# Kernel tuning notes

Hardware: AMD Instinct MI355X
Metric: run time of the kernel (lower is better)

## Reference

```python
import jax, jax.numpy as jnp
import numpy as np

# ViT-B on the Lorentz hyperboloid (curvature C): points x = [x_time, x_space],
# x_time = sqrt(||x_space||^2 + C). All linear/conv/norm ops act on the space
# part and recompute time; residuals/attention-midpoints renormalize the full
# Lorentz vector back onto the hyperboloid.
B, IMG, P, CIN, D, H, L = 32, 224, 16, 3, 768, 12, 12
HD = D // H          # per-head space dim (64)
DFF = 2048           # swiglu hidden: int(2/3 * 4*768) aligned to 64
C = 1.0
EPS = 1e-6


def _time(xs):
    return jnp.sqrt(jnp.clip(jnp.sum(xs * xs, -1, keepdims=True) + C, EPS, None))


def _to_lorentz(xs):
    return jnp.concatenate([_time(xs), xs], -1)


def _project(z):
    # renormalize full Lorentz vector so <z,z>_L = -C
    zz = jnp.sum(z[..., 1:] ** 2, -1, keepdims=True) - z[..., :1] ** 2
    return z * (jnp.sqrt(C) / jnp.sqrt(jnp.clip(-zz, EPS, None)))


def _lorentz_ln(x, g, b):
    xs = x[..., 1:]
    mu = xs.mean(-1, keepdims=True)
    var = ((xs - mu) ** 2).mean(-1, keepdims=True)
    xs = (xs - mu) / jnp.sqrt(var + 1e-6) * g + b
    return _to_lorentz(xs)


def _lresnet(x, y, w):
    # Lorentzian weighted residual: midpoint of x and w*y, projected to manifold
    return _project(x + w * y)


def _rope_tables():
    # 2D axial rope over the 14x14 patch grid, identity rotation for 1 cls token
    n = IMG // P
    d4 = HD // 4
    inv = 1.0 / (100.0 ** (np.arange(d4) / d4))
    ang = np.arange(n)[:, None] * inv[None, :]            # [n, d4]
    ay = np.repeat(ang[:, None, :], n, axis=1)            # row angles
    ax = np.repeat(ang[None, :, :], n, axis=0)            # col angles
    a = np.concatenate([ay, ax], -1).reshape(n * n, HD // 2)
    cos = np.concatenate([np.ones((1, HD // 2)), np.cos(a)], 0)
    sin = np.concatenate([np.zeros((1, HD // 2)), np.sin(a)], 0)
    return jnp.asarray(cos, jnp.float32), jnp.asarray(sin, jnp.float32)


def _apply_rope(x, cos, sin):
    # x: [B,N,H,HD]; rotate consecutive pairs (complex multiply)
    xr = x.reshape(*x.shape[:-1], -1, 2)
    x0, x1 = xr[..., 0], xr[..., 1]
    c = cos[None, :, None, :]
    s = sin[None, :, None, :]
    out = jnp.stack([x0 * c - x1 * s, x0 * s + x1 * c], -1)
    return out.reshape(x.shape)


def _attention(x, Wq, Wk, Wv, Wo, cos, sin, scale):
    b, n, _ = x.shape
    xs = x[..., 1:]
    q = (xs @ Wq).reshape(b, n, H, HD)
    k = (xs @ Wk).reshape(b, n, H, HD)
    v = (xs @ Wv).reshape(b, n, H, HD)
    q = _apply_rope(q, cos, sin)
    k = _apply_rope(k, cos, sin)
    qt = _time(q)[..., 0]   # [B,N,H]
    kt = _time(k)[..., 0]
    # Lorentz inner product <q,k>_L = -q_t k_t + q_s . k_s
    inner = jnp.einsum('bnhd,bmhd->bhnm', q, k) - jnp.einsum('bnh,bmh->bhnm', qt, kt)
    attn = jax.nn.softmax((2.0 * C + 2.0 * inner) / scale, axis=-1)
    vf = jnp.concatenate([_time(v), v], -1)               # [B,M,H,HD+1]
    mid = jnp.einsum('bhnm,bmhe->bnhe', attn, vf)         # Lorentzian midpoint
    mid = _project(mid)
    out_s = mid[..., 1:].reshape(b, n, H * HD) @ Wo       # concat heads + proj
    return _to_lorentz(out_s)


def setup_inputs() -> dict:
    key = jax.random.key(0)
    ks = jax.random.split(key, 12)
    std = 0.02
    nrm = lambda k, shape: jax.random.normal(k, shape, jnp.float32) * std
    return {
        'x': jax.random.normal(ks[0], (B, CIN, IMG, IMG), jnp.float32),
        'cls_s': nrm(ks[1], (D - 1,)),
        'Wp': nrm(ks[2], (P, P, CIN + 1, D - 1)),         # HWIO conv kernel
        'ln1_g': jnp.ones((L, D - 1), jnp.float32),
        'ln1_b': jnp.zeros((L, D - 1), jnp.float32),
        'Wq': nrm(ks[3], (L, D - 1, H * HD)),
        'Wk': nrm(ks[4], (L, D - 1, H * HD)),
        'Wv': nrm(ks[5], (L, D - 1, H * HD)),
        'Wo': nrm(ks[6], (L, H * HD, D - 1)),
        'ln2_g': jnp.ones((L, D - 1), jnp.float32),
        'ln2_b': jnp.zeros((L, D - 1), jnp.float32),
        'W1': nrm(ks[7], (L, D - 1, DFF)),
        'W2': nrm(ks[8], (L, D - 1, DFF)),
        'W3': nrm(ks[9], (L, DFF, D - 1)),
        'wy1': jnp.ones((L,), jnp.float32),
        'wy2': jnp.ones((L,), jnp.float32),
        'lnf_g': jnp.ones((D - 1,), jnp.float32),
        'lnf_b': jnp.zeros((D - 1,), jnp.float32),
    }


def reference(x, cls_s, Wp, ln1_g, ln1_b, Wq, Wk, Wv, Wo, ln2_g, ln2_b,
              W1, W2, W3, wy1, wy2, lnf_g, lnf_b):
    b = x.shape[0]
    xs = jnp.transpose(x, (0, 2, 3, 1))                   # BHWC
    xl = _to_lorentz(xs)                                  # pixel-wise time channel
    feat = jax.lax.conv_general_dilated(
        xl, Wp, (P, P), 'VALID',
        dimension_numbers=('NHWC', 'HWIO', 'NHWC'))       # [B,14,14,D-1]
    tok = _to_lorentz(feat).reshape(b, -1, D)             # [B,196,D]
    cls = jnp.broadcast_to(_to_lorentz(cls_s)[None, None, :], (b, 1, D))
    tok = jnp.concatenate([cls, tok], 1)                  # [B,197,D]
    cos, sin = _rope_tables()
    scale = jnp.sqrt(jnp.asarray(H * HD, jnp.float32))
    for l in range(L):
        xn = _lorentz_ln(tok, ln1_g[l], ln1_b[l])
        a = _attention(xn, Wq[l], Wk[l], Wv[l], Wo[l], cos, sin, scale)
        tok = _lresnet(tok, a, wy1[l])
        xn = _lorentz_ln(tok, ln2_g[l], ln2_b[l])
        hs = xn[..., 1:]
        m = _to_lorentz((jax.nn.silu(hs @ W1[l]) * (hs @ W2[l])) @ W3[l])
        tok = _lresnet(tok, m, wy2[l])
    return _lorentz_ln(tok, lnf_g, lnf_b)
```

## Files before the change

kernel.cpp:

```cpp
#include <hip/hip_runtime.h>
#include <hip/hip_bf16.h>

typedef __attribute__((ext_vector_type(8))) short short8;
typedef __attribute__((ext_vector_type(4))) float f32x4;
typedef _Float16 f16x8 __attribute__((ext_vector_type(8)));

#define NLAYER 12
#define NTOK   6304
#define MPAD   6400
#define CONVM  6272

#define QELE     ((size_t)384*208*64)
#define VELE     ((size_t)384*80*232)

static constexpr size_t AL(size_t x){ return (x + 511) & ~(size_t)511; }
static constexpr size_t B_COS    = 0;
static constexpr size_t B_SIN    = AL(B_COS    + (size_t)197*32*4);
static constexpr size_t B_WPT    = AL(B_SIN    + (size_t)197*32*4);
static constexpr size_t B_APATCH = AL(B_WPT    + (size_t)768*1024*2);
static constexpr size_t B_WQKVT  = AL(B_APATCH + (size_t)CONVM*1024*2);
static constexpr size_t B_WOT    = AL(B_WQKVT  + (size_t)2304*768*2);
static constexpr size_t B_W12T   = AL(B_WOT    + (size_t)768*768*2);
static constexpr size_t B_W3T    = AL(B_W12T   + (size_t)4096*768*2);
static constexpr size_t B_TOK    = AL(B_W3T    + (size_t)768*2048*2);
static constexpr size_t B_ACTA   = AL(B_TOK    + (size_t)NTOK*768*4);
static constexpr size_t B_ACTB   = AL(B_ACTA   + (size_t)MPAD*768*2);
static constexpr size_t B_GOUT   = AL(B_ACTB   + (size_t)MPAD*2048*2);
static constexpr size_t B_QB     = AL(B_GOUT   + (size_t)MPAD*2304*4);
static constexpr size_t B_KB     = AL(B_QB     + QELE*2);
static constexpr size_t B_VT     = AL(B_KB     + QELE*2);
static constexpr size_t B_QTB    = AL(B_VT     + VELE*2);
static constexpr size_t B_KTB    = AL(B_QTB    + (size_t)384*208*4);
static constexpr size_t B_END    = AL(B_KTB    + (size_t)384*208*4);

typedef __attribute__((address_space(1))) unsigned int gu32;
typedef __attribute__((address_space(3))) unsigned int lu32;
__device__ __forceinline__ void gld16(const void* g, void* l) {
  __builtin_amdgcn_global_load_lds((const gu32*)g, (lu32*)l, 16, 0, 0);
}

__device__ __forceinline__ float bsum(float v, float* red) {
  #pragma unroll
  for (int m = 32; m; m >>= 1) v += __shfl_xor(v, m, 64);
  __syncthreads();
  if ((threadIdx.x & 63) == 0) red[threadIdx.x >> 6] = v;
  __syncthreads();
  return red[0] + red[1] + red[2] + red[3];
}

__device__ __forceinline__ ushort h_us(float v) {
  _Float16 h = (_Float16)v;
  return *(ushort*)&h;
}
__device__ __forceinline__ float us_f(ushort u) {
  return (float)*(const _Float16*)&u;
}

__global__ void k_rope_tab(float* __restrict__ cosb, float* __restrict__ sinb) {
  int idx = blockIdx.x * 256 + threadIdx.x;
  if (idx >= 197 * 32) return;
  int p = idx >> 5, j = idx & 31;
  float cv, sv;
  if (p == 0) { cv = 1.f; sv = 0.f; }
  else {
    int pp = p - 1;
    int iy = pp / 14, ix = pp - iy * 14;
    int pos = (j < 16) ? iy : ix;
    int f   = (j < 16) ? j  : j - 16;
    float inv = powf(100.f, -(float)f / 16.f);
    float a = (float)pos * inv;
    cv = cosf(a); sv = sinf(a);
  }
  cosb[idx] = cv; sinb[idx] = sv;
}

__device__ __forceinline__ void tpose_tile(const float* __restrict__ src, ushort* __restrict__ dst,
                                           int K, int N, int ldd, int imode, int tk, int tn) {
  __shared__ float ts[32][33];
  int t = threadIdx.x;
  int rr = t >> 3, c4 = (t & 7) * 4;
  int k0 = tk * 32, n0 = tn * 32;
  #pragma unroll
  for (int e = 0; e < 4; ++e) {
    int k = k0 + rr, n = n0 + c4 + e;
    ts[rr][c4 + e] = (k < K && n < N) ? src[(size_t)k * N + n] : 0.f;
  }
  __syncthreads();
  int c = n0 + rr;
  int drow = (imode == 0) ? c : (16 * (c >> 3) + (c & 7) + (imode == 2 ? 8 : 0));
  ushort4 o;
  #pragma unroll
  for (int e = 0; e < 4; ++e) {
    _Float16 hv = (_Float16)ts[c4 + e][rr];
    ((ushort*)&o)[e] = *(ushort*)&hv;
  }
  *(ushort4*)&dst[(size_t)drow * ldd + k0 + c4] = o;
}

__global__ __launch_bounds__(256) void k_tpose(const float* __restrict__ src, ushort* __restrict__ dst,
                                               int K, int N, int ktiles, int ldd) {
  int tk = blockIdx.x % ktiles, tn = blockIdx.x / ktiles;
  tpose_tile(src, dst, K, N, ldd, 0, tk, tn);
}

__global__ __launch_bounds__(256) void k_wprep(const float* __restrict__ Wq, const float* __restrict__ Wk,
                                               const float* __restrict__ Wv, const float* __restrict__ Wo,
                                               const float* __restrict__ W1, const float* __restrict__ W2,
                                               const float* __restrict__ W3,
                                               ushort* __restrict__ wqkvt, ushort* __restrict__ wot,
                                               ushort* __restrict__ w12t, ushort* __restrict__ w3t) {
  int tile = blockIdx.x;
  const float* src; ushort* dst;
  int K, N, ktiles, ldd, imode = 0, tl;
  if (tile < 2304) {
    int jb = tile / 576; tl = tile % 576;
    ktiles = 24; ldd = 768;
    if (jb == 0)      { src = Wq; dst = wqkvt;                 K = 767; N = 768; }
    else if (jb == 1) { src = Wk; dst = wqkvt + 768 * 768;     K = 767; N = 768; }
    else if (jb == 2) { src = Wv; dst = wqkvt + 2 * 768 * 768; K = 767; N = 768; }
    else              { src = Wo; dst = wot;                   K = 768; N = 767; }
  } else if (tile < 5376) {
    int jb = (tile - 2304) / 1536; tl = (tile - 2304) % 1536;
    ktiles = 24; ldd = 768; K = 767; N = 2048; dst = w12t;
    src = jb ? W2 : W1; imode = jb ? 2 : 1;
  } else {
    tl = tile - 5376; ktiles = 64; ldd = 2048; K = 2048; N = 767; src = W3; dst = w3t;
  }
  int tk = tl % ktiles, tn = tl / ktiles;
  tpose_tile(src, dst, K, N, ldd, imode, tk, tn);
}

__global__ __launch_bounds__(256) void k_im2col(const float* __restrict__ x, ushort* __restrict__ ap) {
  int r = blockIdx.x;
  int b = r / 196, pi = r - b * 196;
  int py = pi / 14, px = pi - py * 14;
  int t = threadIdx.x;
  int ph = t >> 4, pw = t & 15;
  int iy = py * 16 + ph, ix = px * 16 + pw;
  size_t base = ((size_t)b * 3 * 224 + iy) * 224 + ix;
  float x0 = x[base];
  float x1 = x[base + 224 * 224];
  float x2 = x[base + 2 * 224 * 224];
  float tv = sqrtf(fmaxf(x0 * x0 + x1 * x1 + x2 * x2 + 1.f, 1e-6f));
  size_t o = (size_t)r * 1024 + t * 4;
  ap[o] = h_us(tv); ap[o + 1] = h_us(x0); ap[o + 2] = h_us(x1); ap[o + 3] = h_us(x2);
}

template<int MODE>
__global__ __launch_bounds__(256) void k_gemmh(const ushort* __restrict__ A, const ushort* __restrict__ Bt,
                                               float* __restrict__ C, ushort* __restrict__ H,
                                               int N, int K) {
  __shared__ ushort sA[128 * 64];
  __shared__ ushort sB[128 * 64];
  int m0 = blockIdx.x * 128, n0 = blockIdx.y * 128;
  int t = threadIdx.x;
  int w = t >> 6, l = t & 63;
  int wm = (w >> 1) * 64, wn = (w & 1) * 64;
  int lr = l & 15, hi = l >> 4;
  f32x4 acc[4][4] = {};
  for (int k0 = 0; k0 < K; k0 += 64) {
    #pragma unroll
    for (int i = 0; i < 4; ++i) {
      int fl = i * 256 + t;
      int r = fl >> 3, c = fl & 7;
      int cs = c ^ (r & 7);
      gld16(&A[(size_t)(m0 + r) * K + k0 + cs * 8], &sA[fl * 8]);
      gld16(&Bt[(size_t)(n0 + r) * K + k0 + cs * 8], &sB[fl * 8]);
    }
    __syncthreads();
    f16x8 af[4][2], bfr[4][2];
    #pragma unroll
    for (int q = 0; q < 4; ++q) {
      int ra = wm + q * 16 + lr, rb = wn + q * 16 + lr;
      #pragma unroll
      for (int h = 0; h < 2; ++h) {
        af[q][h]  = *(const f16x8*)&sA[ra * 64 + ((h * 4 + hi) ^ (ra & 7)) * 8];
        bfr[q][h] = *(const f16x8*)&sB[rb * 64 + ((h * 4 + hi) ^ (rb & 7)) * 8];
      }
    }
    #pragma unroll
    for (int mi = 0; mi < 4; ++mi)
      #pragma unroll
      for (int ni = 0; ni < 4; ++ni) {
        acc[mi][ni] = __builtin_amdgcn_mfma_f32_16x16x32_f16(af[mi][0], bfr[ni][0], acc[mi][ni], 0, 0, 0);
        acc[mi][ni] = __builtin_amdgcn_mfma_f32_16x16x32_f16(af[mi][1], bfr[ni][1], acc[mi][ni], 0, 0, 0);
      }
    __syncthreads();
  }
  int rr = hi * 4, cc = lr;
  if (MODE == 3) {
    #pragma unroll
    for (int mi = 0; mi < 4; ++mi)
      #pragma unroll
      for (int ni = 0; ni < 4; ++ni)
        #pragma unroll
        for (int j = 0; j < 4; ++j)
          H[(size_t)(m0 + wm + mi * 16 + rr + j) * N + (n0 + wn + ni * 16 + cc)] = h_us(acc[mi][ni][j]);
  } else {
    #pragma unroll
    for (int mi = 0; mi < 4; ++mi)
      #pragma unroll
      for (int ni = 0; ni < 4; ++ni)
        #pragma unroll
        for (int j = 0; j < 4; ++j)
          C[(size_t)(m0 + wm + mi * 16 + rr + j) * N + (n0 + wn + ni * 16 + cc)] = acc[mi][ni][j];
  }
}

template<int MODE>
__global__ __launch_bounds__(512, 2) void k_g256(const ushort* __restrict__ A, const ushort* __restrict__ Bt,
                                                 ushort* __restrict__ H, int N, int K,
                                                 ushort* __restrict__ qbuf, ushort* __restrict__ kbuf,
                                                 ushort* __restrict__ vtb,
                                                 float* __restrict__ qtb, float* __restrict__ ktb,
                                                 const float* __restrict__ cosb, const float* __restrict__ sinb) {
  __shared__ ushort sA[2][2][256 * 32];
  __shared__ ushort sB[2][2][256 * 32];
  const int t = threadIdx.x;
  const int w = t >> 6, l = t & 63;
  const int wr = w >> 2, wc = w & 3;
  const int lr = l & 15, hi4 = l >> 4;
  const int m0 = blockIdx.x * 256, n0 = blockIdx.y * 256;

  auto stageA = [&](int kt, int kh, int buf) {
    #pragma unroll
    for (int ii = 0; ii < 2; ++ii) {
      int q = ii * 512 + t;
      int r = q >> 2, ci = q & 3;
      gld16(&A[(size_t)(m0 + r) * K + kt * 64 + kh * 32 + ((ci ^ ((r >> 1) & 3)) * 8)], &sA[buf][kh][q * 8]);
    }
  };
  auto stageB = [&](int kt, int kh, int buf) {
    #pragma unroll
    for (int ii = 0; ii < 2; ++ii) {
      int q = ii * 512 + t;
      int r = q >> 2, ci = q & 3;
      gld16(&Bt[(size_t)(n0 + r) * K + kt * 64 + kh * 32 + ((ci ^ ((r >> 1) & 3)) * 8)], &sB[buf][kh][q * 8]);
    }
  };

  f32x4 acc[8][4] = {};
  auto ldA = [&](int buf, int ks, int G, f16x8* fr) {
    #pragma unroll
    for (int mi = 0; mi < 4; ++mi) {
      int r = wr * 128 + (G * 4 + mi) * 16 + lr;
      fr[mi] = *(const f16x8*)&sA[buf][ks][(r * 4 + (hi4 ^ ((r >> 1) & 3))) * 8];
    }
  };
  auto ldB = [&](int buf, int ks, f16x8* fr) {
    #pragma unroll
    for (int ni = 0; ni < 4; ++ni) {
      int r = wc * 64 + ni * 16 + lr;
      fr[ni] = *(const f16x8*)&sB[buf][ks][(r * 4 + (hi4 ^ ((r >> 1) & 3))) * 8];
    }
  };
  auto mmaG = [&](int G, f16x8* a, f16x8* b) {
    __builtin_amdgcn_s_setprio(1);
    #pragma unroll
    for (int mi = 0; mi < 4; ++mi)
      #pragma unroll
      for (int ni = 0; ni < 4; ++ni)
        acc[G * 4 + mi][ni] = __builtin_amdgcn_mfma_f32_16x16x32_f16(a[mi], b[ni], acc[G * 4 + mi][ni], 0, 0, 0);
    __builtin_amdgcn_s_setprio(0);
  };

  const int NT = K >> 6;
  const int NI = NT >> 1;
  stageA(0, 0, 0); stageB(0, 0, 0); stageA(0, 1, 0); stageB(0, 1, 0);

  for (int i = 0; i < NI; ++i) {
    const int T1 = 2 * i + 1, T2 = 2 * i + 2;
    const bool last = (i == NI - 1);
    f16x8 a0[4], a1[4], b0[4], b1[4];
    asm volatile("s_waitcnt vmcnt(4)" ::: "memory");
    __builtin_amdgcn_sched_barrier(0);
    __builtin_amdgcn_s_barrier();
    ldA(0, 0, 0, a0); ldB(0, 0, b0);
    stageA(T1, 0, 1);
    mmaG(0, a0, b0);
    ldA(0, 0, 1, a1);
    stageB(T1, 0, 1);
    mmaG(1, a1, b0);
    asm volatile("s_waitcnt vmcnt(4)" ::: "memory");
    __builtin_amdgcn_sched_barrier(0);
    __builtin_amdgcn_s_barrier();
    ldA(0, 1, 0, a0); ldB(0, 1, b1);
    stageA(T1, 1, 1);
    mmaG(0, a0, b1);
    ldA(0, 1, 1, a1);
    stageB(T1, 1, 1);
    mmaG(1, a1, b1);
    asm volatile("s_waitcnt vmcnt(4)" ::: "memory");
    __builtin_amdgcn_sched_barrier(0);
    __builtin_amdgcn_s_barrier();
    ldA(1, 0, 0, a0); ldB(1, 0, b0);
    if (!last) stageA(T2, 0, 0);
    mmaG(0, a0, b0);
    ldA(1, 0, 1, a1);
    if (!last) stageB(T2, 0, 0);
    mmaG(1, a1, b0);
    if (last) { asm volatile("s_waitcnt vmcnt(0)" ::: "memory"); }
    else      { asm volatile("s_waitcnt vmcnt(4)" ::: "memory"); }
    __builtin_amdgcn_sched_barrier(0);
    __builtin_amdgcn_s_barrier();
    ldA(1, 1, 0, a0); ldB(1, 1, b1);
    if (!last) stageA(T2, 1, 0);
    mmaG(0, a0, b1);
    ldA(1, 1, 1, a1);
    if (!last) stageB(T2, 1, 0);
    mmaG(1, a1, b1);
  }

  if (MODE == 1) {
    int cc = lr;
    #pragma unroll
    for (int mi = 0; mi < 8; ++mi)
      #pragma unroll
      for (int ni = 0; ni < 4; ++ni) {
        int g = (n0 + wc * 64 + ni * 16) >> 4;
        #pragma unroll
        for (int j = 0; j < 4; ++j) {
          float v = acc[mi][ni][j];
          float p = __shfl_xor(v, 8);
          float u1 = (cc < 8) ? v : p;
          float u2 = (cc < 8) ? p : v;
          float hv = u1 / (1.f + __expf(-u1)) * u2;
          if (cc < 8)
            H[(size_t)(m0 + wr * 128 + mi * 16 + hi4 * 4 + j) * 2048 + g * 8 + cc] = h_us(hv);
        }
      }
  } else if (MODE == 2) {
    int secBase = n0 + wc * 64;
    int sec = secBase / 768;
    int hh = (secBase - sec * 768) >> 6;
    #pragma unroll
    for (int mi = 0; mi < 8; ++mi) {
      float nrm[4];
      #pragma unroll
      for (int j = 0; j < 4; ++j) {
        float ss = 0.f;
        #pragma unroll
        for (int ni = 0; ni < 4; ++ni) ss += acc[mi][ni][j] * acc[mi][ni][j];
        #pragma unroll
        for (int m = 8; m; m >>= 1) ss += __shfl_xor(ss, m, 64);
        nrm[j] = sqrtf(fmaxf(ss + 1.f, 1e-6f));
      }
      #pragma unroll
      for (int j = 0; j < 4; ++j) {
        int m = m0 + wr * 128 + mi * 16 + hi4 * 4 + j;
        if (m < NTOK) {
          int b = m / 197, nn = m - b * 197;
          int bh = b * 12 + hh;
          if (sec == 2) {
            size_t vo = (size_t)bh * 80 * 232;
            if (lr == 0) vtb[vo + nn] = h_us(nrm[j]);
            #pragma unroll
            for (int ni = 0; ni < 4; ++ni) {
              int e = ni * 16 + lr;
              vtb[vo + (size_t)(1 + e) * 232 + nn] = h_us(acc[mi][ni][j]);
            }
          } else {
            float* tb = (sec == 0) ? qtb : ktb;
            ushort* ob = (sec == 0) ? qbuf : kbuf;
            if (lr == 0) tb[(size_t)bh * 208 + nn] = nrm[j];
            size_t rowb = ((size_t)bh * 208 + nn) * 64;
            #pragma unroll
            for (int ni = 0; ni < 4; ++ni) {
              int d = ni * 16 + lr;
              float v = acc[mi][ni][j];
              float p = __shfl_xor(v, 1);
              int j2 = d >> 1;
              float cz = cosb[nn * 32 + j2], sz = sinb[nn * 32 + j2];
              float rv = ((lr & 1) == 0) ? (v * cz - p * sz) : (p * sz + v * cz);
              ob[rowb + d] = h_us(rv);
            }
          }
        }
      }
    }
  }
}

__global__ __launch_bounds__(256) void k_build_tok(const float* __restrict__ feat, const float* __restrict__ cls,
                                                   float* __restrict__ tok) {
  __shared__ float red[8];
  int r = blockIdx.x;
  int b = r / 197, i = r - b * 197;
  int t = threadIdx.x;
  const float* src = (i == 0) ? cls : (feat + (size_t)(b * 196 + i - 1) * 768);
  float v0 = src[t], v1 = src[256 + t], v2 = (t < 255) ? src[512 + t] : 0.f;
  float qs = bsum(v0 * v0 + v1 * v1 + v2 * v2, red);
  float* tp = tok + (size_t)r * 768;
  if (t == 0) tp[0] = sqrtf(fmaxf(qs + 1.f, 1e-6f));
  tp[1 + t] = v0; tp[257 + t] = v1; if (t < 255) tp[513 + t] = v2;
}

__global__ __launch_bounds__(256) void k_ln(const float* __restrict__ tok, const float* __restrict__ g,
                                            const float* __restrict__ bb, ushort* __restrict__ out) {
  __shared__ float red[8];
  int r = blockIdx.x, t = threadIdx.x;
  const float* xp = tok + (size_t)r * 768;
  float v0 = xp[1 + t], v1 = xp[257 + t], v2 = (t < 255) ? xp[513 + t] : 0.f;
  float s = bsum(v0 + v1 + v2, red);
  float q = bsum(v0 * v0 + v1 * v1 + v2 * v2, red);
  float mu = s * (1.f / 767.f);
  float rstd = rsqrtf(fmaxf(q * (1.f / 767.f) - mu * mu, 0.f) + 1e-6f);
  size_t o = (size_t)r * 768;
  out[o + t]       = h_us((v0 - mu) * rstd * g[t]       + bb[t]);
  out[o + 256 + t] = h_us((v1 - mu) * rstd * g[256 + t] + bb[256 + t]);
  if (t < 255)
    out[o + 512 + t] = h_us((v2 - mu) * rstd * g[512 + t] + bb[512 + t]);
  if (t == 255) out[o + 767] = 0;
}

__global__ __launch_bounds__(128) void k_attn(const ushort* __restrict__ qbuf,
                                              const float* __restrict__ qtb,
                                              const ushort* __restrict__ kbuf,
                                              const float* __restrict__ ktb,
                                              const ushort* __restrict__ vtb,
                                              ushort* __restrict__ outa) {
  __shared__ ushort sK[208 * 72];
  __shared__ ushort sP[2][16 * 248];
  __shared__ float  sKt[208];
  int half = blockIdx.x, bh = blockIdx.y;
  int b = bh / 12, hd = bh - b * 12;
  int t = threadIdx.x, w = t >> 6, l = t & 63;
  const ushort* kg = kbuf + (size_t)bh * 208 * 64;
  for (int cks = t; cks < 1664; cks += 128) {
    int r = cks >> 3, c8 = (cks & 7) * 8;
    *(int4*)&sK[r * 72 + c8] = *(const int4*)&kg[r * 64 + c8];
  }
  for (int i = t; i < 208; i += 128) sKt[i] = ktb[(size_t)bh * 208 + i];
  __syncthreads();
  const ushort* qg = qbuf + (size_t)bh * 208 * 64;
  const ushort* vg = vtb + (size_t)bh * 80 * 232;
  const float invs = 0.03608439182435161f;
  int rt0 = half ? 7 : 0, rt1 = half ? 13 : 7;
  int lr = l & 15, hi4 = l >> 4;
  ushort* pw = &sP[w][0];
  for (int rt = rt0 + w; rt < rt1; rt += 2) {
    int qrow = (rt * 16 + lr) * 64 + hi4 * 8;
    f16x8 q0 = *(const f16x8*)&qg[qrow];
    f16x8 q1 = *(const f16x8*)&qg[qrow + 32];
    float qt4[4];
    #pragma unroll
    for (int j = 0; j < 4; ++j) qt4[j] = qtb[(size_t)bh * 208 + rt * 16 + hi4 * 4 + j];
    f32x4 acc[13];
    #pragma unroll
    for (int nt = 0; nt < 13; ++nt) {
      int kr = (nt * 16 + lr) * 72 + hi4 * 8;
      f16x8 k0 = *(const f16x8*)&sK[kr];
      f16x8 k1 = *(const f16x8*)&sK[kr + 32];
      acc[nt] = (f32x4){0.f, 0.f, 0.f, 0.f};
      acc[nt] = __builtin_amdgcn_mfma_f32_16x16x32_f16(q0, k0, acc[nt], 0, 0, 0);
      acc[nt] = __builtin_amdgcn_mfma_f32_16x16x32_f16(q1, k1, acc[nt], 0, 0, 0);
    }
    float mx[4] = {-1e30f, -1e30f, -1e30f, -1e30f};
    #pragma unroll
    for (int nt = 0; nt < 13; ++nt) {
      int cI = nt * 16 + lr;
      float ktc = sKt[cI];
      bool valid = (cI < 197);
      #pragma unroll
      for (int j = 0; j < 4; ++j) {
        float s = (2.f + 2.f * (acc[nt][j] - qt4[j] * ktc)) * invs;
        acc[nt][j] = s;
        if (valid) mx[j] = fmaxf(mx[j], s);
      }
    }
    #pragma unroll
    for (int j = 0; j < 4; ++j)
      #pragma unroll
      for (int m = 8; m; m >>= 1) mx[j] = fmaxf(mx[j], __shfl_xor(mx[j], m, 64));
    #pragma unroll
    for (int nt = 0; nt < 14; ++nt) {
      int cI = nt * 16 + lr;
      #pragma unroll
      for (int j = 0; j < 4; ++j) {
        float p = (nt < 13 && cI < 197) ? __expf(acc[nt][j] - mx[j]) : 0.f;
        pw[(hi4 * 4 + j) * 248 + cI] = h_us(p);
      }
    }
    f32x4 accO[5];
    #pragma unroll
    for (int et = 0; et < 5; ++et) accO[et] = (f32x4){0.f, 0.f, 0.f, 0.f};
    #pragma unroll
    for (int ks = 0; ks < 7; ++ks) {
      f16x8 pa = *(const f16x8*)&pw[lr * 248 + ks * 32 + hi4 * 8];
      #pragma unroll
      for (int et = 0; et < 5; ++et) {
        int er = et * 16 + lr;
        f16x8 bv = *(const f16x8*)&vg[(er > 64 ? 64 : er) * 232 + ks * 32 + hi4 * 8];
        accO[et] = __builtin_amdgcn_mfma_f32_16x16x32_f16(pa, bv, accO[et], 0, 0, 0);
      }
    }
    float ssq[4] = {0.f, 0.f, 0.f, 0.f};
    #pragma unroll
    for (int et = 0; et < 4; ++et)
      #pragma unroll
      for (int j = 0; j < 4; ++j) ssq[j] += accO[et][j] * accO[et][j];
    if (lr == 0) {
      #pragma unroll
      for (int j = 0; j < 4; ++j) ssq[j] += accO[4][j] * accO[4][j];
    }
    #pragma unroll
    for (int j = 0; j < 4; ++j)
      #pragma unroll
      for (int m = 8; m; m >>= 1) ssq[j] += __shfl_xor(ssq[j], m, 64);
    float rf4[4];
    #pragma unroll
    for (int j = 0; j < 4; ++j) {
      float o0 = __shfl(accO[0][j], (l & 48));
      rf4[j] = rsqrtf(fmaxf(2.f * o0 * o0 - ssq[j], 1e-6f));
    }
    #pragma unroll
    for (int et = 0; et < 5; ++et) {
      int e = et * 16 + lr;
      if (e == 0 || e >= 65) continue;
      #pragma unroll
      for (int j = 0; j < 4; ++j) {
        int n = rt * 16 + hi4 * 4 + j;
        if (n < 197)
          outa[((size_t)(b * 197 + n)) * 768 + hd * 64 + (e - 1)] = h_us(accO[et][j] * rf4[j]);
      }
    }
  }
}

template<int FIN>
__global__ __launch_bounds__(256) void k_resnet_ln(float* __restrict__ tok, const ushort* __restrict__ s,
                                                   const float* __restrict__ wyp, int l,
                                                   const float* __restrict__ g, const float* __restrict__ bb,
                                                   ushort* __restrict__ out16, float* __restrict__ out32) {
  __shared__ float red[8];
  __shared__ float bc[1];
  int r = blockIdx.x, t = threadIdx.x;
  float w = wyp[l];
  const ushort* sp = s + (size_t)r * 768;
  float* tp = tok + (size_t)r * 768;
  float s0 = us_f(sp[t]), s1 = us_f(sp[256 + t]), s2 = (t < 255) ? us_f(sp[512 + t]) : 0.f;
  float qs = bsum(s0 * s0 + s1 * s1 + s2 * s2, red);
  float at = sqrtf(fmaxf(qs + 1.f, 1e-6f));
  float z0 = tp[1 + t] + w * s0;
  float z1 = tp[257 + t] + w * s1;
  float z2 = (t < 255) ? (tp[513 + t] + w * s2) : 0.f;
  float zs = bsum(z0 * z0 + z1 * z1 + z2 * z2, red);
  if (t == 0) bc[0] = tp[0] + w * at;
  __syncthreads();
  float zt = bc[0];
  float rf = rsqrtf(fmaxf(zt * zt - zs, 1e-6f));
  float n0 = z0 * rf, n1 = z1 * rf, n2 = z2 * rf;
  tp[1 + t] = n0; tp[257 + t] = n1; if (t < 255) tp[513 + t] = n2;
  if (t == 0) tp[0] = zt * rf;
  float sm = bsum(n0 + n1 + n2, red);
  float sq = bsum(n0 * n0 + n1 * n1 + n2 * n2, red);
  float mu = sm * (1.f / 767.f);
  float rstd = rsqrtf(fmaxf(sq * (1.f / 767.f) - mu * mu, 0.f) + 1e-6f);
  float y0 = (n0 - mu) * rstd * g[t] + bb[t];
  float y1 = (n1 - mu) * rstd * g[256 + t] + bb[256 + t];
  float y2 = (t < 255) ? ((n2 - mu) * rstd * g[512 + t] + bb[512 + t]) : 0.f;
  if (FIN) {
    float qq = bsum(y0 * y0 + y1 * y1 + y2 * y2, red);
    float* op = out32 + (size_t)r * 768;
    op[1 + t] = y0; op[257 + t] = y1; if (t < 255) op[513 + t] = y2;
    if (t == 0) op[0] = sqrtf(fmaxf(qq + 1.f, 1e-6f));
  } else {
    size_t o = (size_t)r * 768;
    out16[o + t] = h_us(y0);
    out16[o + 256 + t] = h_us(y1);
    if (t < 255) out16[o + 512 + t] = h_us(y2);
    if (t == 255) out16[o + 767] = 0;
  }
}

extern "C" void kernel_launch(void* const* d_in, const int* in_sizes, int n_in,
                              void* d_out, int out_size, void* d_ws, size_t ws_size,
                              hipStream_t stream) {
  const float* x     = (const float*)d_in[0];
  const float* cls_s = (const float*)d_in[1];
  const float* Wp    = (const float*)d_in[2];
  const float* ln1g  = (const float*)d_in[3];
  const float* ln1b  = (const float*)d_in[4];
  const float* Wq    = (const float*)d_in[5];
  const float* Wk    = (const float*)d_in[6];
  const float* Wv    = (const float*)d_in[7];
  const float* Wo    = (const float*)d_in[8];
  const float* ln2g  = (const float*)d_in[9];
  const float* ln2b  = (const float*)d_in[10];
  const float* W1    = (const float*)d_in[11];
  const float* W2    = (const float*)d_in[12];
  const float* W3    = (const float*)d_in[13];
  const float* wy1   = (const float*)d_in[14];
  const float* wy2   = (const float*)d_in[15];
  const float* lnfg  = (const float*)d_in[16];
  const float* lnfb  = (const float*)d_in[17];

  if (ws_size < B_END) return;

  char* ws = (char*)d_ws;
  float*  cosb   = (float*)(ws + B_COS);
  float*  sinb   = (float*)(ws + B_SIN);
  ushort* wpt    = (ushort*)(ws + B_WPT);
  ushort* apatch = (ushort*)(ws + B_APATCH);
  ushort* wqkvt  = (ushort*)(ws + B_WQKVT);
  ushort* wot    = (ushort*)(ws + B_WOT);
  ushort* w12t   = (ushort*)(ws + B_W12T);
  ushort* w3t    = (ushort*)(ws + B_W3T);
  float*  tok    = (float*)(ws + B_TOK);
  ushort* acta   = (ushort*)(ws + B_ACTA);
  ushort* actb   = (ushort*)(ws + B_ACTB);
  float*  gout   = (float*)(ws + B_GOUT);
  ushort* gouth  = (ushort*)(ws + B_GOUT);
  ushort* qbuf   = (ushort*)(ws + B_QB);
  ushort* kbuf   = (ushort*)(ws + B_KB);
  ushort* vtb    = (ushort*)(ws + B_VT);
  float*  qtb    = (float*)(ws + B_QTB);
  float*  ktb    = (float*)(ws + B_KTB);

  hipMemsetAsync(vtb, 0, VELE * 2, stream);

  k_rope_tab<<<25, 256, 0, stream>>>(cosb, sinb);
  k_tpose<<<32 * 24, 256, 0, stream>>>(Wp, wpt, 1024, 767, 32, 1024);
  k_im2col<<<CONVM, 256, 0, stream>>>(x, apatch);
  k_gemmh<0><<<dim3(49, 6), 256, 0, stream>>>(apatch, wpt, gout, nullptr, 768, 1024);
  k_build_tok<<<NTOK, 256, 0, stream>>>(gout, cls_s, tok);
  k_ln<<<NTOK, 256, 0, stream>>>(tok, ln1g, ln1b, acta);

  for (int l = 0; l < NLAYER; ++l) {
    k_wprep<<<6912, 256, 0, stream>>>(Wq + (size_t)l * 767 * 768, Wk + (size_t)l * 767 * 768,
                                      Wv + (size_t)l * 767 * 768, Wo + (size_t)l * 768 * 767,
                                      W1 + (size_t)l * 767 * 2048, W2 + (size_t)l * 767 * 2048,
                                      W3 + (size_t)l * 2048 * 767, wqkvt, wot, w12t, w3t);

    k_g256<2><<<dim3(25, 9), 512, 0, stream>>>(acta, wqkvt, nullptr, 2304, 768,
                                               qbuf, kbuf, vtb, qtb, ktb, cosb, sinb);
    k_attn<<<dim3(2, 384), 128, 0, stream>>>(qbuf, qtb, kbuf, ktb, vtb, acta);
    k_gemmh<3><<<dim3(50, 6), 256, 0, stream>>>(acta, wot, nullptr, gouth, 768, 768);
    k_resnet_ln<0><<<NTOK, 256, 0, stream>>>(tok, gouth, wy1, l,
                                             ln2g + (size_t)l * 767, ln2b + (size_t)l * 767, acta, nullptr);

    k_g256<1><<<dim3(25, 16), 512, 0, stream>>>(acta, w12t, actb, 4096, 768,
                                                nullptr, nullptr, nullptr, nullptr, nullptr, nullptr, nullptr);
    k_gemmh<3><<<dim3(50, 6), 256, 0, stream>>>(actb, w3t, nullptr, gouth, 768, 2048);
    if (l < NLAYER - 1)
      k_resnet_ln<0><<<NTOK, 256, 0, stream>>>(tok, gouth, wy2, l,
                                               ln1g + (size_t)(l + 1) * 767, ln1b + (size_t)(l + 1) * 767,
                                               acta, nullptr);
    else
      k_resnet_ln<1><<<NTOK, 256, 0, stream>>>(tok, gouth, wy2, l, lnfg, lnfb, nullptr, (float*)d_out);
  }
}
```

Measured before the change: 3.274 ms.

## Remap GEMM blocks across XCDs, move SwiGLU GEMM to 128-tile kernel, split attention per row tile

Adds an XCD-aware block index remap to both GEMM kernels so that consecutive tiles land on the same XCD and share L2. The W1/W2 SwiGLU GEMM moves from the 256x256 double-buffered kernel to the simpler 128x128 kernel, which gives a larger grid. The attention kernel drops LDS staging of K and launches one wave per 16-row tile across seven blocks, reading K and its time component directly from global memory. The aim is better L2 locality and occupancy, at the cost of less data reuse from LDS and a less pipelined GEMM for the largest matmul.

```diff
diff --git a/kernel.cpp b/kernel.cpp
--- a/kernel.cpp
+++ b/kernel.cpp
@@ -54,6 +54,17 @@
 }
 __device__ __forceinline__ float us_f(ushort u) {
   return (float)*(const _Float16*)&u;
+}
+
+__device__ __forceinline__ void xcd_remap(int& bx, int& by) {
+  int gx = gridDim.x, gy = gridDim.y;
+  int nwg = gx * gy;
+  int orig = blockIdx.y * gx + blockIdx.x;
+  int q = nwg >> 3, r = nwg & 7;
+  int xcd = orig & 7, loc = orig >> 3;
+  int wg = (xcd < r ? xcd * (q + 1) : r * (q + 1) + (xcd - r) * q) + loc;
+  bx = wg / gy;
+  by = wg % gy;
 }
 
 __global__ void k_rope_tab(float* __restrict__ cosb, float* __restrict__ sinb) {
@@ -152,7 +163,9 @@
                                                int N, int K) {
   __shared__ ushort sA[128 * 64];
   __shared__ ushort sB[128 * 64];
-  int m0 = blockIdx.x * 128, n0 = blockIdx.y * 128;
+  int bx, by;
+  xcd_remap(bx, by);
+  int m0 = bx * 128, n0 = by * 128;
   int t = threadIdx.x;
   int w = t >> 6, l = t & 63;
   int wm = (w >> 1) * 64, wn = (w & 1) * 64;
@@ -188,7 +201,24 @@
     __syncthreads();
   }
   int rr = hi * 4, cc = lr;
-  if (MODE == 3) {
+  if (MODE == 1) {
+    #pragma unroll
+    for (int mi = 0; mi < 4; ++mi)
+      #pragma unroll
+      for (int ni = 0; ni < 4; ++ni) {
+        int g = (n0 + wn + ni * 16) >> 4;
+        #pragma unroll
+        for (int j = 0; j < 4; ++j) {
+          float v = acc[mi][ni][j];
+          float p = __shfl_xor(v, 8);
+          float u1 = (cc < 8) ? v : p;
+          float u2 = (cc < 8) ? p : v;
+          float hv = u1 / (1.f + __expf(-u1)) * u2;
+          if (cc < 8)
+            H[(size_t)(m0 + wm + mi * 16 + rr + j) * 2048 + g * 8 + cc] = h_us(hv);
+        }
+      }
+  } else if (MODE == 3) {
     #pragma unroll
     for (int mi = 0; mi < 4; ++mi)
       #pragma unroll
@@ -220,7 +250,9 @@
   const int w = t >> 6, l = t & 63;
   const int wr = w >> 2, wc = w & 3;
   const int lr = l & 15, hi4 = l >> 4;
-  const int m0 = blockIdx.x * 256, n0 = blockIdx.y * 256;
+  int bx, by;
+  xcd_remap(bx, by);
+  const int m0 = bx * 256, n0 = by * 256;
 
   auto stageA = [&](int kt, int kh, int buf) {
     #pragma unroll
@@ -311,25 +343,7 @@
     mmaG(1, a1, b1);
   }
 
-  if (MODE == 1) {
-    int cc = lr;
-    #pragma unroll
-    for (int mi = 0; mi < 8; ++mi)
-      #pragma unroll
-      for (int ni = 0; ni < 4; ++ni) {
-        int g = (n0 + wc * 64 + ni * 16) >> 4;
-        #pragma unroll
-        for (int j = 0; j < 4; ++j) {
-          float v = acc[mi][ni][j];
-          float p = __shfl_xor(v, 8);
-          float u1 = (cc < 8) ? v : p;
-          float u2 = (cc < 8) ? p : v;
-          float hv = u1 / (1.f + __expf(-u1)) * u2;
-          if (cc < 8)
-            H[(size_t)(m0 + wr * 128 + mi * 16 + hi4 * 4 + j) * 2048 + g * 8 + cc] = h_us(hv);
-        }
-      }
-  } else if (MODE == 2) {
+  if (MODE == 2) {
     int secBase = n0 + wc * 64;
     int sec = secBase / 768;
     int hh = (secBase - sec * 768) >> 6;
@@ -419,110 +433,103 @@
                                               const float* __restrict__ ktb,
                                               const ushort* __restrict__ vtb,
                                               ushort* __restrict__ outa) {
-  __shared__ ushort sK[208 * 72];
   __shared__ ushort sP[2][16 * 248];
-  __shared__ float  sKt[208];
-  int half = blockIdx.x, bh = blockIdx.y;
+  int bxt = blockIdx.x, bh = blockIdx.y;
   int b = bh / 12, hd = bh - b * 12;
   int t = threadIdx.x, w = t >> 6, l = t & 63;
+  int rt = bxt * 2 + w;
+  if (rt >= 13) return;
+  int lr = l & 15, hi4 = l >> 4;
+  const ushort* qg = qbuf + (size_t)bh * 208 * 64;
   const ushort* kg = kbuf + (size_t)bh * 208 * 64;
-  for (int cks = t; cks < 1664; cks += 128) {
-    int r = cks >> 3, c8 = (cks & 7) * 8;
-    *(int4*)&sK[r * 72 + c8] = *(const int4*)&kg[r * 64 + c8];
-  }
-  for (int i = t; i < 208; i += 128) sKt[i] = ktb[(size_t)bh * 208 + i];
-  __syncthreads();
-  const ushort* qg = qbuf + (size_t)bh * 208 * 64;
   const ushort* vg = vtb + (size_t)bh * 80 * 232;
+  const float*  ktp = ktb + (size_t)bh * 208;
   const float invs = 0.03608439182435161f;
-  int rt0 = half ? 7 : 0, rt1 = half ? 13 : 7;
-  int lr = l & 15, hi4 = l >> 4;
   ushort* pw = &sP[w][0];
-  for (int rt = rt0 + w; rt < rt1; rt += 2) {
-    int qrow = (rt * 16 + lr) * 64 + hi4 * 8;
-    f16x8 q0 = *(const f16x8*)&qg[qrow];
-    f16x8 q1 = *(const f16x8*)&qg[qrow + 32];
-    float qt4[4];
-    #pragma unroll
-    for (int j = 0; j < 4; ++j) qt4[j] = qtb[(size_t)bh * 208 + rt * 16 + hi4 * 4 + j];
-    f32x4 acc[13];
-    #pragma unroll
-    for (int nt = 0; nt < 13; ++nt) {
-      int kr = (nt * 16 + lr) * 72 + hi4 * 8;
-      f16x8 k0 = *(const f16x8*)&sK[kr];
-      f16x8 k1 = *(const f16x8*)&sK[kr + 32];
-      acc[nt] = (f32x4){0.f, 0.f, 0.f, 0.f};
-      acc[nt] = __builtin_amdgcn_mfma_f32_16x16x32_f16(q0, k0, acc[nt], 0, 0, 0);
-      acc[nt] = __builtin_amdgcn_mfma_f32_16x16x32_f16(q1, k1, acc[nt], 0, 0, 0);
-    }
-    float mx[4] = {-1e30f, -1e30f, -1e30f, -1e30f};
-    #pragma unroll
-    for (int nt = 0; nt < 13; ++nt) {
-      int cI = nt * 16 + lr;
-      float ktc = sKt[cI];
-      bool valid = (cI < 197);
-      #pragma unroll
-      for (int j = 0; j < 4; ++j) {
-        float s = (2.f + 2.f * (acc[nt][j] - qt4[j] * ktc)) * invs;
-        acc[nt][j] = s;
-        if (valid) mx[j] = fmaxf(mx[j], s);
-      }
-    }
-    #pragma unroll
-    for (int j = 0; j < 4; ++j)
-      #pragma unroll
-      for (int m = 8; m; m >>= 1) mx[j] = fmaxf(mx[j], __shfl_xor(mx[j], m, 64));
-    #pragma unroll
-    for (int nt = 0; nt < 14; ++nt) {
-      int cI = nt * 16 + lr;
-      #pragma unroll
-      for (int j = 0; j < 4; ++j) {
-        float p = (nt < 13 && cI < 197) ? __expf(acc[nt][j] - mx[j]) : 0.f;
-        pw[(hi4 * 4 + j) * 248 + cI] = h_us(p);
-      }
-    }
-    f32x4 accO[5];
-    #pragma unroll
-    for (int et = 0; et < 5; ++et) accO[et] = (f32x4){0.f, 0.f, 0.f, 0.f};
-    #pragma unroll
-    for (int ks = 0; ks < 7; ++ks) {
-      f16x8 pa = *(const f16x8*)&pw[lr * 248 + ks * 32 + hi4 * 8];
-      #pragma unroll
-      for (int et = 0; et < 5; ++et) {
-        int er = et * 16 + lr;
-        f16x8 bv = *(const f16x8*)&vg[(er > 64 ? 64 : er) * 232 + ks * 32 + hi4 * 8];
-        accO[et] = __builtin_amdgcn_mfma_f32_16x16x32_f16(pa, bv, accO[et], 0, 0, 0);
-      }
-    }
-    float ssq[4] = {0.f, 0.f, 0.f, 0.f};
-    #pragma unroll
-    for (int et = 0; et < 4; ++et)
-      #pragma unroll
-      for (int j = 0; j < 4; ++j) ssq[j] += accO[et][j] * accO[et][j];
-    if (lr == 0) {
-      #pragma unroll
-      for (int j = 0; j < 4; ++j) ssq[j] += accO[4][j] * accO[4][j];
-    }
-    #pragma unroll
-    for (int j = 0; j < 4; ++j)
-      #pragma unroll
-      for (int m = 8; m; m >>= 1) ssq[j] += __shfl_xor(ssq[j], m, 64);
-    float rf4[4];
+
+  int qrow = (rt * 16 + lr) * 64 + hi4 * 8;
+  f16x8 q0 = *(const f16x8*)&qg[qrow];
+  f16x8 q1 = *(const f16x8*)&qg[qrow + 32];
+  float qt4[4];
+  #pragma unroll
+  for (int j = 0; j < 4; ++j) qt4[j] = qtb[(size_t)bh * 208 + rt * 16 + hi4 * 4 + j];
+  f32x4 acc[13];
+  #pragma unroll
+  for (int nt = 0; nt < 13; ++nt) {
+    int kr = (nt * 16 + lr) * 64 + hi4 * 8;
+    f16x8 k0 = *(const f16x8*)&kg[kr];
+    f16x8 k1 = *(const f16x8*)&kg[kr + 32];
+    acc[nt] = (f32x4){0.f, 0.f, 0.f, 0.f};
+    acc[nt] = __builtin_amdgcn_mfma_f32_16x16x32_f16(q0, k0, acc[nt], 0, 0, 0);
+    acc[nt] = __builtin_amdgcn_mfma_f32_16x16x32_f16(q1, k1, acc[nt], 0, 0, 0);
+  }
+  float mx[4] = {-1e30f, -1e30f, -1e30f, -1e30f};
+  #pragma unroll
+  for (int nt = 0; nt < 13; ++nt) {
+    int cI = nt * 16 + lr;
+    float ktc = ktp[cI];
+    bool valid = (cI < 197);
     #pragma unroll
     for (int j = 0; j < 4; ++j) {
-      float o0 = __shfl(accO[0][j], (l & 48));
-      rf4[j] = rsqrtf(fmaxf(2.f * o0 * o0 - ssq[j], 1e-6f));
-    }
+      float s = (2.f + 2.f * (acc[nt][j] - qt4[j] * ktc)) * invs;
+      acc[nt][j] = s;
+      if (valid) mx[j] = fmaxf(mx[j], s);
+    }
+  }
+  #pragma unroll
+  for (int j = 0; j < 4; ++j)
+    #pragma unroll
+    for (int m = 8; m; m >>= 1) mx[j] = fmaxf(mx[j], __shfl_xor(mx[j], m, 64));
+  #pragma unroll
+  for (int nt = 0; nt < 14; ++nt) {
+    int cI = nt * 16 + lr;
+    #pragma unroll
+    for (int j = 0; j < 4; ++j) {
+      float p = (nt < 13 && cI < 197) ? __expf(acc[nt][j] - mx[j]) : 0.f;
+      pw[(hi4 * 4 + j) * 248 + cI] = h_us(p);
+    }
+  }
+  f32x4 accO[5];
+  #pragma unroll
+  for (int et = 0; et < 5; ++et) accO[et] = (f32x4){0.f, 0.f, 0.f, 0.f};
+  #pragma unroll
+  for (int ks = 0; ks < 7; ++ks) {
+    f16x8 pa = *(const f16x8*)&pw[lr * 248 + ks * 32 + hi4 * 8];
     #pragma unroll
     for (int et = 0; et < 5; ++et) {
-      int e = et * 16 + lr;
-      if (e == 0 || e >= 65) continue;
-      #pragma unroll
-      for (int j = 0; j < 4; ++j) {
-        int n = rt * 16 + hi4 * 4 + j;
-        if (n < 197)
-          outa[((size_t)(b * 197 + n)) * 768 + hd * 64 + (e - 1)] = h_us(accO[et][j] * rf4[j]);
-      }
+      int er = et * 16 + lr;
+      f16x8 bv = *(const f16x8*)&vg[(er > 64 ? 64 : er) * 232 + ks * 32 + hi4 * 8];
+      accO[et] = __builtin_amdgcn_mfma_f32_16x16x32_f16(pa, bv, accO[et], 0, 0, 0);
+    }
+  }
+  float ssq[4] = {0.f, 0.f, 0.f, 0.f};
+  #pragma unroll
+  for (int et = 0; et < 4; ++et)
+    #pragma unroll
+    for (int j = 0; j < 4; ++j) ssq[j] += accO[et][j] * accO[et][j];
+  if (lr == 0) {
+    #pragma unroll
+    for (int j = 0; j < 4; ++j) ssq[j] += accO[4][j] * accO[4][j];
+  }
+  #pragma unroll
+  for (int j = 0; j < 4; ++j)
+    #pragma unroll
+    for (int m = 8; m; m >>= 1) ssq[j] += __shfl_xor(ssq[j], m, 64);
+  float rf4[4];
+  #pragma unroll
+  for (int j = 0; j < 4; ++j) {
+    float o0 = __shfl(accO[0][j], (l & 48));
+    rf4[j] = rsqrtf(fmaxf(2.f * o0 * o0 - ssq[j], 1e-6f));
+  }
+  #pragma unroll
+  for (int et = 0; et < 5; ++et) {
+    int e = et * 16 + lr;
+    if (e == 0 || e >= 65) continue;
+    #pragma unroll
+    for (int j = 0; j < 4; ++j) {
+      int n = rt * 16 + hi4 * 4 + j;
+      if (n < 197)
+        outa[((size_t)(b * 197 + n)) * 768 + hd * 64 + (e - 1)] = h_us(accO[et][j] * rf4[j]);
     }
   }
 }
@@ -634,13 +641,12 @@
 
     k_g256<2><<<dim3(25, 9), 512, 0, stream>>>(acta, wqkvt, nullptr, 2304, 768,
                                                qbuf, kbuf, vtb, qtb, ktb, cosb, sinb);
-    k_attn<<<dim3(2, 384), 128, 0, stream>>>(qbuf, qtb, kbuf, ktb, vtb, acta);
+    k_attn<<<dim3(7, 384), 128, 0, stream>>>(qbuf, qtb, kbuf, ktb, vtb, acta);
     k_gemmh<3><<<dim3(50, 6), 256, 0, stream>>>(acta, wot, nullptr, gouth, 768, 768);
     k_resnet_ln<0><<<NTOK, 256, 0, stream>>>(tok, gouth, wy1, l,
                                              ln2g + (size_t)l * 767, ln2b + (size_t)l * 767, acta, nullptr);
 
-    k_g256<1><<<dim3(25, 16), 512, 0, stream>>>(acta, w12t, actb, 4096, 768,
-                                                nullptr, nullptr, nullptr, nullptr, nullptr, nullptr, nullptr);
+    k_gemmh<1><<<dim3(50, 32), 256, 0, stream>>>(acta, w12t, nullptr, actb, 4096, 768);
     k_gemmh<3><<<dim3(50, 6), 256, 0, stream>>>(actb, w3t, nullptr, gouth, 768, 2048);
     if (l < NLAYER - 1)
       k_resnet_ln<0><<<NTOK, 256, 0, stream>>>(tok, gouth, wy2, l,
```

Result: faster. 3.156 ms (-3.6%).
